# Performance work log

Hardware: AMD Instinct MI355X
Metric: run time of the kernel (lower is better)

The kernel has to match this reference:

```python
import jax, jax.numpy as jnp
import numpy as np

N_USERS = 100000
N_ITEMS = 50000
N = N_USERS + N_ITEMS
EMB = 64
NNZ = 8000000
N_LAYERS = 3


def setup_inputs() -> dict:
    key = jax.random.key(0)
    k1, k2, k3, k4, k5 = jax.random.split(key, 5)
    user_emb = jax.random.normal(k1, (N_USERS, EMB), dtype=jnp.float32) * 0.1
    item_emb = jax.random.normal(k2, (N_ITEMS, EMB), dtype=jnp.float32) * 0.1
    adj_rows = jax.random.randint(k3, (NNZ,), 0, N, dtype=jnp.int32)
    adj_cols = jax.random.randint(k4, (NNZ,), 0, N, dtype=jnp.int32)
    # normalized-adjacency-like small positive values
    adj_vals = jax.random.uniform(k5, (NNZ,), dtype=jnp.float32) * 0.01
    return {
        "user_emb": user_emb,
        "item_emb": item_emb,
        "adj_rows": adj_rows,
        "adj_cols": adj_cols,
        "adj_vals": adj_vals,
    }


def spmm(rows, cols, vals, x):
    # sparse [N,N] @ dense [N,d]: gather source rows, scale, scatter-add to dest
    msgs = vals[:, None] * x[cols]          # [nnz, d]
    return jax.ops.segment_sum(msgs, rows, num_segments=N)  # [N, d]


def reference(user_emb, item_emb, adj_rows, adj_cols, adj_vals):
    ego = jnp.concatenate([user_emb, item_emb], axis=0)  # [N, d]
    acc = ego  # running sum of layer outputs (fused stack+mean)
    for _ in range(N_LAYERS):
        ego = spmm(adj_rows, adj_cols, adj_vals, ego)
        acc = acc + ego
    all_embeddings = acc / jnp.float32(N_LAYERS + 1)
    return all_embeddings[:N_USERS], all_embeddings[N_USERS:]
```

## Files before the change

kernel.cpp:

```cpp
#include <hip/hip_runtime.h>

#define N_USERS 100000
#define N_ITEMS 50000
#define N_TOTAL 150000
#define EMB 64
#define NNZ_CONST 8000000

#define CB_SHIFT 8
#define ROWS_PER_CB 256
#define NCB 586
#define CAP_R 14592
#define EPB 8192

#define CHUNK_SHIFT 15
#define NCHUNK 5
#define KBINS (NCHUNK * ROWS_PER_CB)
#define CRNG_STRIDE 1312

#define VAL_ENC 1638400.0f
#define VAL_DEC 2.3841858e-9f
#define FP8_SCALE 256.0f

typedef unsigned char u8;
typedef unsigned short u16;
typedef unsigned int u32;
typedef unsigned long long u64;
typedef float v2f __attribute__((ext_vector_type(2)));

__device__ __forceinline__ u16 f32_to_bf16(float f) {
    u32 b = __float_as_uint(f);
    b += 0x7FFFu + ((b >> 16) & 1u);
    return (u16)(b >> 16);
}
__device__ __forceinline__ float bf16lo_to_f32(u32 w) {
    return __uint_as_float(w << 16);
}
__device__ __forceinline__ float bf16hi_to_f32(u32 w) {
    return __uint_as_float(w & 0xFFFF0000u);
}
__device__ __forceinline__ u32 pack_bf16x2(float lo, float hi) {
    return ((u32)f32_to_bf16(hi) << 16) | f32_to_bf16(lo);
}
__device__ __forceinline__ u32 pack_fp8x4(float a, float b, float c, float d) {
    u32 r = (u32)__builtin_amdgcn_cvt_pk_fp8_f32(a, b, 0, false);
    r = (u32)__builtin_amdgcn_cvt_pk_fp8_f32(c, d, (int)r, true);
    return r;
}

__global__ void lgcn_init_kernel(const float* __restrict__ user_emb,
                                 const float* __restrict__ item_emb,
                                 float* __restrict__ acc,
                                 u8* __restrict__ ego8) {
    const long total4 = (long)N_TOTAL * EMB / 4;
    long idx = (long)blockIdx.x * blockDim.x + threadIdx.x;
    if (idx >= total4) return;
    long e = idx * 4;
    const long user_elems = (long)N_USERS * EMB;
    float4 v;
    if (e < user_elems) {
        v = *(const float4*)(user_emb + e);
    } else {
        v = *(const float4*)(item_emb + (e - user_elems));
    }
    *(float4*)(acc + e) = v;
    *(u32*)(ego8 + e) = pack_fp8x4(v.x * FP8_SCALE, v.y * FP8_SCALE,
                                   v.z * FP8_SCALE, v.w * FP8_SCALE);
}

__global__ void lgcn_gcinit_kernel(int* __restrict__ gcursor) {
    int t = blockIdx.x * blockDim.x + threadIdx.x;
    if (t < NCB) gcursor[t] = t * CAP_R;
}

__global__ void __launch_bounds__(512) lgcn_part_kernel(
        const int* __restrict__ rows,
        const int* __restrict__ cols,
        const float* __restrict__ vals,
        int* __restrict__ gcursor,
        u32* __restrict__ pairs,
        u8* __restrict__ rl8) {
    __shared__ u32 stage32[EPB];
    __shared__ u8  stage8[EPB];
    __shared__ int lhist[NCB];
    __shared__ int loffs[NCB + 1];
    __shared__ int lcur[NCB];
    __shared__ int gres[NCB];
    const int t = threadIdx.x;
    const long base = (long)blockIdx.x * EPB;
    long rem = (long)NNZ_CONST - base;
    const int n = (rem < EPB) ? (int)rem : EPB;
    const int n4 = n >> 2;

    for (int i = t; i < NCB; i += 512) lhist[i] = 0;
    __syncthreads();

    for (int i4 = t; i4 < n4; i4 += 512) {
        int4 r = *(const int4*)(rows + base + (long)i4 * 4);
        atomicAdd(&lhist[r.x >> CB_SHIFT], 1);
        atomicAdd(&lhist[r.y >> CB_SHIFT], 1);
        atomicAdd(&lhist[r.z >> CB_SHIFT], 1);
        atomicAdd(&lhist[r.w >> CB_SHIFT], 1);
    }
    __syncthreads();

    if (t < 64) {
        int loc[10];
        int s = 0;
        #pragma unroll
        for (int k = 0; k < 10; ++k) {
            int i = t * 10 + k;
            loc[k] = (i < NCB) ? lhist[i] : 0;
            s += loc[k];
        }
        int inc = s;
        #pragma unroll
        for (int d = 1; d < 64; d <<= 1) {
            int u = __shfl_up(inc, d, 64);
            if (t >= d) inc += u;
        }
        int ex = inc - s;
        #pragma unroll
        for (int k = 0; k < 10; ++k) {
            int i = t * 10 + k;
            if (i < NCB) { loffs[i] = ex; lcur[i] = ex; ex += loc[k]; }
        }
        if (t == 63) loffs[NCB] = ex;
    }
    __syncthreads();

    for (int i = t; i < NCB; i += 512) {
        int c = lhist[i];
        gres[i] = c ? atomicAdd(&gcursor[i], c) : 0;
    }
    __syncthreads();

    for (int i4 = t; i4 < n4; i4 += 512) {
        int4 r = *(const int4*)(rows + base + (long)i4 * 4);
        int4 c = *(const int4*)(cols + base + (long)i4 * 4);
        float4 v = *(const float4*)(vals + base + (long)i4 * 4);
#define PUTL(RR, CC, VV)                                                \
        {                                                               \
            const int cb = (RR) >> CB_SHIFT;                            \
            int pos = atomicAdd(&lcur[cb], 1);                          \
            int k14 = (int)((VV) * VAL_ENC + 0.5f);                     \
            if (k14 > 16383) k14 = 16383;                               \
            stage32[pos] = ((u32)k14 << 18) | (u32)(CC);                \
            stage8[pos] = (u8)((RR) & (ROWS_PER_CB - 1));               \
        }
        PUTL(r.x, c.x, v.x)
        PUTL(r.y, c.y, v.y)
        PUTL(r.z, c.z, v.z)
        PUTL(r.w, c.w, v.w)
#undef PUTL
    }
    __syncthreads();

    for (int i = t; i < n; i += 512) {
        int lo = 0, hi = NCB;
        while (hi - lo > 1) {
            int mid = (lo + hi) >> 1;
            if (loffs[mid] <= i) lo = mid; else hi = mid;
        }
        long d = (long)gres[lo] + (i - loffs[lo]);
        pairs[d] = stage32[i];
        rl8[d] = stage8[i];
    }
}

__global__ void __launch_bounds__(512) lgcn_csort_kernel(
        const int* __restrict__ gcursor,
        const u8* __restrict__ rl8,
        u32* __restrict__ pairs,
        int* __restrict__ crng) {
    __shared__ u32 stage[CAP_R];
    __shared__ int khist[KBINS];
    __shared__ int kcur[KBINS];
    const int b = blockIdx.x;
    const int t = threadIdx.x;
    const long gbase = (long)b * CAP_R;
    const int cbase = b * CRNG_STRIDE;
    int n = gcursor[b] - (int)gbase;
    if (n < 0) n = 0;
    if (n > CAP_R) n = CAP_R;

    for (int i = t; i < KBINS; i += 512) khist[i] = 0;
    __syncthreads();

    for (int i = t; i < n; i += 512) {
        u32 p = pairs[gbase + i];
        int key = (int)((p & 0x3FFFFu) >> CHUNK_SHIFT) * ROWS_PER_CB
                + (int)rl8[gbase + i];
        atomicAdd(&khist[key], 1);
    }
    __syncthreads();

    if (t < 64) {
        int loc[20];
        int s = 0;
        #pragma unroll
        for (int k = 0; k < 20; ++k) {
            loc[k] = khist[t * 20 + k];
            s += loc[k];
        }
        int inc = s;
        #pragma unroll
        for (int d = 1; d < 64; d <<= 1) {
            int u = __shfl_up(inc, d, 64);
            if (t >= d) inc += u;
        }
        int ex = inc - s;
        #pragma unroll
        for (int k = 0; k < 20; ++k) {
            kcur[t * 20 + k] = ex;
            crng[cbase + t * 20 + k] = (int)gbase + ex;
            ex += loc[k];
        }
        if (t == 63) crng[cbase + KBINS] = (int)gbase + ex;
    }
    __syncthreads();

    for (int i = t; i < n; i += 512) {
        u32 p = pairs[gbase + i];
        int key = (int)((p & 0x3FFFFu) >> CHUNK_SHIFT) * ROWS_PER_CB
                + (int)rl8[gbase + i];
        int pos = atomicAdd(&kcur[key], 1);
        stage[pos] = p;
    }
    __syncthreads();

    for (int i = t; i < n; i += 512)
        pairs[gbase + i] = stage[i];
}

template <bool WFP8>
__global__ void __launch_bounds__(256) lgcn_spmm_kernel(
        const int* __restrict__ crng,
        const u32* __restrict__ pairs,
        const u8* __restrict__ src8,
        u8* __restrict__ dst8,
        u16* __restrict__ dst_bf16) {
    const int t = threadIdx.x;
    const int bucket = blockIdx.x >> 1;
    const int rbase = (blockIdx.x & 1) * 128;
    const int g  = t >> 3;
    const int l8 = t & 7;
    const u8* srcl = src8 + l8 * 8;
    const int cbase = bucket * CRNG_STRIDE;

    v2f a00 = {0.f,0.f}, a01 = {0.f,0.f}, a02 = {0.f,0.f}, a03 = {0.f,0.f};
    v2f a10 = {0.f,0.f}, a11 = {0.f,0.f}, a12 = {0.f,0.f}, a13 = {0.f,0.f};
    v2f a20 = {0.f,0.f}, a21 = {0.f,0.f}, a22 = {0.f,0.f}, a23 = {0.f,0.f};
    v2f a30 = {0.f,0.f}, a31 = {0.f,0.f}, a32 = {0.f,0.f}, a33 = {0.f,0.f};

#define PROCS(I, S, F, Q0, Q1, Q2, Q3)                                      \
    {                                                                       \
        const int ii = (S) + (I);                                           \
        const bool ok = ii < (F);                                           \
        const u32 p = pairs[ok ? ii : 0];                                   \
        const int c = (int)(p & 0x3FFFFu);                                  \
        const float v = ok ? (float)(p >> 18) * VAL_DEC : 0.0f;             \
        const uint2 x = *(const uint2*)(srcl + ((size_t)c << 6));           \
        const v2f vv = {v, v};                                              \
        Q0 += vv * __builtin_amdgcn_cvt_pk_f32_fp8(x.x, false);             \
        Q1 += vv * __builtin_amdgcn_cvt_pk_f32_fp8(x.x, true);              \
        Q2 += vv * __builtin_amdgcn_cvt_pk_f32_fp8(x.y, false);             \
        Q3 += vv * __builtin_amdgcn_cvt_pk_f32_fp8(x.y, true);              \
    }
#define STEP(I)                                                             \
    PROCS(I, s0, f0, a00, a01, a02, a03)                                    \
    PROCS(I, s1, f1, a10, a11, a12, a13)                                    \
    PROCS(I, s2, f2, a20, a21, a22, a23)                                    \
    PROCS(I, s3, f3, a30, a31, a32, a33)

    for (int k = 0; k < NCHUNK; ++k) {
        const int key0 = cbase + (k << 8) + rbase + g;
        const int s0 = crng[key0];      const int f0 = crng[key0 + 1];
        const int s1 = crng[key0 + 32]; const int f1 = crng[key0 + 33];
        const int s2 = crng[key0 + 64]; const int f2 = crng[key0 + 65];
        const int s3 = crng[key0 + 96]; const int f3 = crng[key0 + 97];
        const int len = max(max(f0 - s0, f1 - s1), max(f2 - s2, f3 - s3));
        int i = 0;
        for (; i + 1 < len; i += 2) {
            STEP(i)
            STEP(i + 1)
        }
        if (i < len) STEP(i)
        __syncthreads();
    }
#undef STEP
#undef PROCS

#define WRITE(J, Q0, Q1, Q2, Q3)                                            \
    {                                                                       \
        const int grow = bucket * ROWS_PER_CB + rbase + g + 32 * (J);       \
        if (grow < N_TOTAL) {                                               \
            const size_t o = (size_t)grow * EMB + l8 * 8;                   \
            uint4 h;                                                        \
            h.x = pack_bf16x2(Q0.x, Q0.y);                                  \
            h.y = pack_bf16x2(Q1.x, Q1.y);                                  \
            h.z = pack_bf16x2(Q2.x, Q2.y);                                  \
            h.w = pack_bf16x2(Q3.x, Q3.y);                                  \
            *(uint4*)(dst_bf16 + o) = h;                                    \
            if (WFP8) {                                                     \
                uint2 q;                                                    \
                q.x = pack_fp8x4(Q0.x * FP8_SCALE, Q0.y * FP8_SCALE,        \
                                 Q1.x * FP8_SCALE, Q1.y * FP8_SCALE);       \
                q.y = pack_fp8x4(Q2.x * FP8_SCALE, Q2.y * FP8_SCALE,        \
                                 Q3.x * FP8_SCALE, Q3.y * FP8_SCALE);       \
                *(uint2*)(dst8 + o) = q;                                    \
            }                                                               \
        }                                                                   \
    }

    WRITE(0, a00, a01, a02, a03)
    WRITE(1, a10, a11, a12, a13)
    WRITE(2, a20, a21, a22, a23)
    WRITE(3, a30, a31, a32, a33)
#undef WRITE
}

__global__ void lgcn_merge_kernel(float* __restrict__ acc,
                                  const u16* __restrict__ e1,
                                  const u16* __restrict__ e2,
                                  const u16* __restrict__ e3) {
    const long total8 = (long)N_TOTAL * EMB / 8;
    long idx = (long)blockIdx.x * blockDim.x + threadIdx.x;
    if (idx >= total8) return;
    long o = idx * 8;
    float4 x0 = *(const float4*)(acc + o);
    float4 x1 = *(const float4*)(acc + o + 4);
    const uint4 h1 = *(const uint4*)(e1 + o);
    const uint4 h2 = *(const uint4*)(e2 + o);
    const uint4 h3 = *(const uint4*)(e3 + o);
    x0.x = (x0.x + bf16lo_to_f32(h1.x) + bf16lo_to_f32(h2.x) + bf16lo_to_f32(h3.x)) * 0.25f;
    x0.y = (x0.y + bf16hi_to_f32(h1.x) + bf16hi_to_f32(h2.x) + bf16hi_to_f32(h3.x)) * 0.25f;
    x0.z = (x0.z + bf16lo_to_f32(h1.y) + bf16lo_to_f32(h2.y) + bf16lo_to_f32(h3.y)) * 0.25f;
    x0.w = (x0.w + bf16hi_to_f32(h1.y) + bf16hi_to_f32(h2.y) + bf16hi_to_f32(h3.y)) * 0.25f;
    x1.x = (x1.x + bf16lo_to_f32(h1.z) + bf16lo_to_f32(h2.z) + bf16lo_to_f32(h3.z)) * 0.25f;
    x1.y = (x1.y + bf16hi_to_f32(h1.z) + bf16hi_to_f32(h2.z) + bf16hi_to_f32(h3.z)) * 0.25f;
    x1.z = (x1.z + bf16lo_to_f32(h1.w) + bf16lo_to_f32(h2.w) + bf16lo_to_f32(h3.w)) * 0.25f;
    x1.w = (x1.w + bf16hi_to_f32(h1.w) + bf16hi_to_f32(h2.w) + bf16hi_to_f32(h3.w)) * 0.25f;
    *(float4*)(acc + o) = x0;
    *(float4*)(acc + o + 4) = x1;
}

extern "C" void kernel_launch(void* const* d_in, const int* in_sizes, int n_in,
                              void* d_out, int out_size, void* d_ws, size_t ws_size,
                              hipStream_t stream) {
    const float* user_emb = (const float*)d_in[0];
    const float* item_emb = (const float*)d_in[1];
    const int*   adj_rows = (const int*)d_in[2];
    const int*   adj_cols = (const int*)d_in[3];
    const float* adj_vals = (const float*)d_in[4];

    float* acc = (float*)d_out;

    char* ws = (char*)d_ws;
    u8* fp8A = (u8*)ws;             ws += (size_t)N_TOTAL * EMB;
    u8* fp8B = (u8*)ws;             ws += (size_t)N_TOTAL * EMB;
    u16* e1 = (u16*)ws;             ws += (size_t)N_TOTAL * EMB * 2;
    u16* e2 = (u16*)ws;             ws += (size_t)N_TOTAL * EMB * 2;
    u16* e3 = (u16*)ws;             ws += (size_t)N_TOTAL * EMB * 2;
    u32* pairs = (u32*)ws;          ws += (size_t)NCB * CAP_R * 4;
    u8* rl8 = (u8*)ws;              ws += (size_t)NCB * CAP_R;
    int* crng = (int*)ws;           ws += (size_t)NCB * CRNG_STRIDE * 4;
    int* gcursor = (int*)ws;        ws += (size_t)(NCB + 8) * 4;

    const int block = 256;
    const long total4 = (long)N_TOTAL * EMB / 4;
    const int grid_elem = (int)((total4 + block - 1) / block);

    lgcn_init_kernel<<<grid_elem, block, 0, stream>>>(user_emb, item_emb, acc, fp8A);

    lgcn_gcinit_kernel<<<(NCB + 255) / 256, 256, 0, stream>>>(gcursor);
    const int grid_part = (NNZ_CONST + EPB - 1) / EPB;
    lgcn_part_kernel<<<grid_part, 512, 0, stream>>>(adj_rows, adj_cols, adj_vals,
                                                    gcursor, pairs, rl8);
    lgcn_csort_kernel<<<NCB, 512, 0, stream>>>(gcursor, rl8, pairs, crng);

    const int grid_spmm = NCB * 2;
    lgcn_spmm_kernel<true><<<grid_spmm, block, 0, stream>>>(crng, pairs, fp8A, fp8B, e1);
    lgcn_spmm_kernel<true><<<grid_spmm, block, 0, stream>>>(crng, pairs, fp8B, fp8A, e2);
    lgcn_spmm_kernel<false><<<grid_spmm, block, 0, stream>>>(crng, pairs, fp8A, fp8B, e3);

    const long total8 = (long)N_TOTAL * EMB / 8;
    const int grid_merge = (int)((total8 + block - 1) / block);
    lgcn_merge_kernel<<<grid_merge, block, 0, stream>>>(acc, e1, e2, e3);
}
```

Before: 444.4 us.

## Gather bf16 embeddings instead of fp8 and fuse final merge into last SpMM

```diff
diff --git a/kernel.cpp b/kernel.cpp
--- a/kernel.cpp
+++ b/kernel.cpp
@@ -18,8 +18,7 @@
 #define CRNG_STRIDE 1312
 
 #define VAL_ENC 1638400.0f
-#define VAL_DEC 2.3841858e-9f
-#define FP8_SCALE 256.0f
+#define VAL_DEC 6.1035156e-7f
 
 typedef unsigned char u8;
 typedef unsigned short u16;
@@ -41,16 +40,11 @@
 __device__ __forceinline__ u32 pack_bf16x2(float lo, float hi) {
     return ((u32)f32_to_bf16(hi) << 16) | f32_to_bf16(lo);
 }
-__device__ __forceinline__ u32 pack_fp8x4(float a, float b, float c, float d) {
-    u32 r = (u32)__builtin_amdgcn_cvt_pk_fp8_f32(a, b, 0, false);
-    r = (u32)__builtin_amdgcn_cvt_pk_fp8_f32(c, d, (int)r, true);
-    return r;
-}
 
 __global__ void lgcn_init_kernel(const float* __restrict__ user_emb,
                                  const float* __restrict__ item_emb,
                                  float* __restrict__ acc,
-                                 u8* __restrict__ ego8) {
+                                 u16* __restrict__ ego_bf16) {
     const long total4 = (long)N_TOTAL * EMB / 4;
     long idx = (long)blockIdx.x * blockDim.x + threadIdx.x;
     if (idx >= total4) return;
@@ -63,8 +57,10 @@
         v = *(const float4*)(item_emb + (e - user_elems));
     }
     *(float4*)(acc + e) = v;
-    *(u32*)(ego8 + e) = pack_fp8x4(v.x * FP8_SCALE, v.y * FP8_SCALE,
-                                   v.z * FP8_SCALE, v.w * FP8_SCALE);
+    uint2 h;
+    h.x = pack_bf16x2(v.x, v.y);
+    h.y = pack_bf16x2(v.z, v.w);
+    *(uint2*)(ego_bf16 + e) = h;
 }
 
 __global__ void lgcn_gcinit_kernel(int* __restrict__ gcursor) {
@@ -232,19 +228,21 @@
         pairs[gbase + i] = stage[i];
 }
 
-template <bool WFP8>
+template <bool MERGE>
 __global__ void __launch_bounds__(256) lgcn_spmm_kernel(
         const int* __restrict__ crng,
         const u32* __restrict__ pairs,
-        const u8* __restrict__ src8,
-        u8* __restrict__ dst8,
-        u16* __restrict__ dst_bf16) {
+        const u16* __restrict__ src,
+        u16* __restrict__ dst,
+        const u16* __restrict__ e1,
+        const u16* __restrict__ e2,
+        float* __restrict__ acc) {
     const int t = threadIdx.x;
     const int bucket = blockIdx.x >> 1;
     const int rbase = (blockIdx.x & 1) * 128;
     const int g  = t >> 3;
     const int l8 = t & 7;
-    const u8* srcl = src8 + l8 * 8;
+    const u16* srcl = src + l8 * 8;
     const int cbase = bucket * CRNG_STRIDE;
 
     v2f a00 = {0.f,0.f}, a01 = {0.f,0.f}, a02 = {0.f,0.f}, a03 = {0.f,0.f};
@@ -259,12 +257,12 @@
         const u32 p = pairs[ok ? ii : 0];                                   \
         const int c = (int)(p & 0x3FFFFu);                                  \
         const float v = ok ? (float)(p >> 18) * VAL_DEC : 0.0f;             \
-        const uint2 x = *(const uint2*)(srcl + ((size_t)c << 6));           \
+        const uint4 x = *(const uint4*)(srcl + ((size_t)c << 6));           \
         const v2f vv = {v, v};                                              \
-        Q0 += vv * __builtin_amdgcn_cvt_pk_f32_fp8(x.x, false);             \
-        Q1 += vv * __builtin_amdgcn_cvt_pk_f32_fp8(x.x, true);              \
-        Q2 += vv * __builtin_amdgcn_cvt_pk_f32_fp8(x.y, false);             \
-        Q3 += vv * __builtin_amdgcn_cvt_pk_f32_fp8(x.y, true);              \
+        Q0 += vv * (v2f){bf16lo_to_f32(x.x), bf16hi_to_f32(x.x)};           \
+        Q1 += vv * (v2f){bf16lo_to_f32(x.y), bf16hi_to_f32(x.y)};           \
+        Q2 += vv * (v2f){bf16lo_to_f32(x.z), bf16hi_to_f32(x.z)};           \
+        Q3 += vv * (v2f){bf16lo_to_f32(x.w), bf16hi_to_f32(x.w)};           \
     }
 #define STEP(I)                                                             \
     PROCS(I, s0, f0, a00, a01, a02, a03)                                    \
@@ -295,19 +293,28 @@
         const int grow = bucket * ROWS_PER_CB + rbase + g + 32 * (J);       \
         if (grow < N_TOTAL) {                                               \
             const size_t o = (size_t)grow * EMB + l8 * 8;                   \
-            uint4 h;                                                        \
-            h.x = pack_bf16x2(Q0.x, Q0.y);                                  \
-            h.y = pack_bf16x2(Q1.x, Q1.y);                                  \
-            h.z = pack_bf16x2(Q2.x, Q2.y);                                  \
-            h.w = pack_bf16x2(Q3.x, Q3.y);                                  \
-            *(uint4*)(dst_bf16 + o) = h;                                    \
-            if (WFP8) {                                                     \
-                uint2 q;                                                    \
-                q.x = pack_fp8x4(Q0.x * FP8_SCALE, Q0.y * FP8_SCALE,        \
-                                 Q1.x * FP8_SCALE, Q1.y * FP8_SCALE);       \
-                q.y = pack_fp8x4(Q2.x * FP8_SCALE, Q2.y * FP8_SCALE,        \
-                                 Q3.x * FP8_SCALE, Q3.y * FP8_SCALE);       \
-                *(uint2*)(dst8 + o) = q;                                    \
+            if (MERGE) {                                                    \
+                const uint4 h1 = *(const uint4*)(e1 + o);                   \
+                const uint4 h2 = *(const uint4*)(e2 + o);                   \
+                float4 x0 = *(const float4*)(acc + o);                      \
+                float4 x1 = *(const float4*)(acc + o + 4);                  \
+                x0.x = (x0.x + bf16lo_to_f32(h1.x) + bf16lo_to_f32(h2.x) + Q0.x) * 0.25f; \
+                x0.y = (x0.y + bf16hi_to_f32(h1.x) + bf16hi_to_f32(h2.x) + Q0.y) * 0.25f; \
+                x0.z = (x0.z + bf16lo_to_f32(h1.y) + bf16lo_to_f32(h2.y) + Q1.x) * 0.25f; \
+                x0.w = (x0.w + bf16hi_to_f32(h1.y) + bf16hi_to_f32(h2.y) + Q1.y) * 0.25f; \
+                x1.x = (x1.x + bf16lo_to_f32(h1.z) + bf16lo_to_f32(h2.z) + Q2.x) * 0.25f; \
+                x1.y = (x1.y + bf16hi_to_f32(h1.z) + bf16hi_to_f32(h2.z) + Q2.y) * 0.25f; \
+                x1.z = (x1.z + bf16lo_to_f32(h1.w) + bf16lo_to_f32(h2.w) + Q3.x) * 0.25f; \
+                x1.w = (x1.w + bf16hi_to_f32(h1.w) + bf16hi_to_f32(h2.w) + Q3.y) * 0.25f; \
+                *(float4*)(acc + o) = x0;                                   \
+                *(float4*)(acc + o + 4) = x1;                               \
+            } else {                                                        \
+                uint4 h;                                                    \
+                h.x = pack_bf16x2(Q0.x, Q0.y);                              \
+                h.y = pack_bf16x2(Q1.x, Q1.y);                              \
+                h.z = pack_bf16x2(Q2.x, Q2.y);                              \
+                h.w = pack_bf16x2(Q3.x, Q3.y);                              \
+                *(uint4*)(dst + o) = h;                                     \
             }                                                               \
         }                                                                   \
     }
@@ -317,31 +324,6 @@
     WRITE(2, a20, a21, a22, a23)
     WRITE(3, a30, a31, a32, a33)
 #undef WRITE
-}
-
-__global__ void lgcn_merge_kernel(float* __restrict__ acc,
-                                  const u16* __restrict__ e1,
-                                  const u16* __restrict__ e2,
-                                  const u16* __restrict__ e3) {
-    const long total8 = (long)N_TOTAL * EMB / 8;
-    long idx = (long)blockIdx.x * blockDim.x + threadIdx.x;
-    if (idx >= total8) return;
-    long o = idx * 8;
-    float4 x0 = *(const float4*)(acc + o);
-    float4 x1 = *(const float4*)(acc + o + 4);
-    const uint4 h1 = *(const uint4*)(e1 + o);
-    const uint4 h2 = *(const uint4*)(e2 + o);
-    const uint4 h3 = *(const uint4*)(e3 + o);
-    x0.x = (x0.x + bf16lo_to_f32(h1.x) + bf16lo_to_f32(h2.x) + bf16lo_to_f32(h3.x)) * 0.25f;
-    x0.y = (x0.y + bf16hi_to_f32(h1.x) + bf16hi_to_f32(h2.x) + bf16hi_to_f32(h3.x)) * 0.25f;
-    x0.z = (x0.z + bf16lo_to_f32(h1.y) + bf16lo_to_f32(h2.y) + bf16lo_to_f32(h3.y)) * 0.25f;
-    x0.w = (x0.w + bf16hi_to_f32(h1.y) + bf16hi_to_f32(h2.y) + bf16hi_to_f32(h3.y)) * 0.25f;
-    x1.x = (x1.x + bf16lo_to_f32(h1.z) + bf16lo_to_f32(h2.z) + bf16lo_to_f32(h3.z)) * 0.25f;
-    x1.y = (x1.y + bf16hi_to_f32(h1.z) + bf16hi_to_f32(h2.z) + bf16hi_to_f32(h3.z)) * 0.25f;
-    x1.z = (x1.z + bf16lo_to_f32(h1.w) + bf16lo_to_f32(h2.w) + bf16lo_to_f32(h3.w)) * 0.25f;
-    x1.w = (x1.w + bf16hi_to_f32(h1.w) + bf16hi_to_f32(h2.w) + bf16hi_to_f32(h3.w)) * 0.25f;
-    *(float4*)(acc + o) = x0;
-    *(float4*)(acc + o + 4) = x1;
 }
 
 extern "C" void kernel_launch(void* const* d_in, const int* in_sizes, int n_in,
@@ -356,11 +338,9 @@
     float* acc = (float*)d_out;
 
     char* ws = (char*)d_ws;
-    u8* fp8A = (u8*)ws;             ws += (size_t)N_TOTAL * EMB;
-    u8* fp8B = (u8*)ws;             ws += (size_t)N_TOTAL * EMB;
+    u16* ego0 = (u16*)ws;           ws += (size_t)N_TOTAL * EMB * 2;
     u16* e1 = (u16*)ws;             ws += (size_t)N_TOTAL * EMB * 2;
     u16* e2 = (u16*)ws;             ws += (size_t)N_TOTAL * EMB * 2;
-    u16* e3 = (u16*)ws;             ws += (size_t)N_TOTAL * EMB * 2;
     u32* pairs = (u32*)ws;          ws += (size_t)NCB * CAP_R * 4;
     u8* rl8 = (u8*)ws;              ws += (size_t)NCB * CAP_R;
     int* crng = (int*)ws;           ws += (size_t)NCB * CRNG_STRIDE * 4;
@@ -370,7 +350,7 @@
     const long total4 = (long)N_TOTAL * EMB / 4;
     const int grid_elem = (int)((total4 + block - 1) / block);
 
-    lgcn_init_kernel<<<grid_elem, block, 0, stream>>>(user_emb, item_emb, acc, fp8A);
+    lgcn_init_kernel<<<grid_elem, block, 0, stream>>>(user_emb, item_emb, acc, ego0);
 
     lgcn_gcinit_kernel<<<(NCB + 255) / 256, 256, 0, stream>>>(gcursor);
     const int grid_part = (NNZ_CONST + EPB - 1) / EPB;
@@ -379,11 +359,10 @@
     lgcn_csort_kernel<<<NCB, 512, 0, stream>>>(gcursor, rl8, pairs, crng);
 
     const int grid_spmm = NCB * 2;
-    lgcn_spmm_kernel<true><<<grid_spmm, block, 0, stream>>>(crng, pairs, fp8A, fp8B, e1);
-    lgcn_spmm_kernel<true><<<grid_spmm, block, 0, stream>>>(crng, pairs, fp8B, fp8A, e2);
-    lgcn_spmm_kernel<false><<<grid_spmm, block, 0, stream>>>(crng, pairs, fp8A, fp8B, e3);
-
-    const long total8 = (long)N_TOTAL * EMB / 8;
-    const int grid_merge = (int)((total8 + block - 1) / block);
-    lgcn_merge_kernel<<<grid_merge, block, 0, stream>>>(acc, e1, e2, e3);
-}
+    lgcn_spmm_kernel<false><<<grid_spmm, block, 0, stream>>>(
+        crng, pairs, ego0, e1, nullptr, nullptr, nullptr);
+    lgcn_spmm_kernel<false><<<grid_spmm, block, 0, stream>>>(
+        crng, pairs, e1, e2, nullptr, nullptr, nullptr);
+    lgcn_spmm_kernel<true><<<grid_spmm, block, 0, stream>>>(
+        crng, pairs, e2, nullptr, e1, e2, acc);
+}
```

After: 505.1 us. 13.7% more time.
